# Performance work log

Hardware: AMD Instinct MI355X
Metric: run time of the kernel (lower is better)

## Reference

```python
import jax, jax.numpy as jnp
import numpy as np
import math

B, S, D = 4, 2048, 768
H = 12
DH = D // H  # 64
NEG = -1e10

def setup_inputs() -> dict:
    key = jax.random.key(0)
    ks = jax.random.split(key, 8)
    scale = 0.02
    return {
        "hidden_states": jax.random.normal(ks[0], (B, S, D), dtype=jnp.float32),
        "attention_mask": jnp.zeros((B, 1, 1, S), dtype=jnp.float32),
        "Wq": jax.random.normal(ks[1], (D, D), dtype=jnp.float32) * scale,
        "bq": jnp.zeros((D,), dtype=jnp.float32),
        "Wk": jax.random.normal(ks[2], (D, D), dtype=jnp.float32) * scale,
        "bk": jnp.zeros((D,), dtype=jnp.float32),
        "Wv": jax.random.normal(ks[3], (D, D), dtype=jnp.float32) * scale,
        "bv": jnp.zeros((D,), dtype=jnp.float32),
    }

def reference(hidden_states, attention_mask, Wq, bq, Wk, bk, Wv, bv):
    # Linear projections; note attention_mask is accepted but unused, matching the torch module.
    def split_heads(x):  # [B,S,D] -> [B,H,S,DH]
        return x.reshape(B, S, H, DH).transpose(0, 2, 1, 3)
    q = split_heads(hidden_states @ Wq + bq)
    k = split_heads(hidden_states @ Wk + bk)
    v = split_heads(hidden_states @ Wv + bv)
    scores = jnp.einsum("bhqd,bhkd->bhqk", q, k) / math.sqrt(DH)
    causal = jnp.tril(jnp.ones((S, S), dtype=bool))  # masked_fill(mask==0, -1e10)
    scores = jnp.where(causal, scores, NEG)
    probs = jax.nn.softmax(scores, axis=-1)
    # dropout prob = 0.0 (eval) -> identity
    ctx = jnp.einsum("bhqk,bhkd->bhqd", probs, v)
    return ctx.transpose(0, 2, 1, 3).reshape(B, S, D)
```

## Files before the change

### kernel.cpp

```cpp
#include <hip/hip_runtime.h>
#include <hip/hip_bf16.h>

#define B_  4
#define S_  2048
#define D_  768
#define H_  12
#define DH_ 64

typedef __bf16 bf16;
typedef __attribute__((ext_vector_type(8))) __bf16 bf16x8;
typedef __attribute__((ext_vector_type(4))) __bf16 bf16x4;
typedef __attribute__((ext_vector_type(4))) float floatx4;

__device__ __forceinline__ int chunk_off(int qt) {
    if (qt < 8)  return qt;
    if (qt < 16) return 8 + 2 * (qt - 8);
    if (qt < 24) return 24 + 3 * (qt - 16);
    return 48 + 4 * (qt - 24);
}

__global__ __launch_bounds__(256) void cvt_f32_bf16(const float* __restrict__ in,
                                                    bf16* __restrict__ out, int n4) {
    int i = blockIdx.x * 256 + threadIdx.x;
    if (i < n4) {
        float4 v = ((const float4*)in)[i];
        bf16x4 o;
        o[0] = (bf16)v.x; o[1] = (bf16)v.y; o[2] = (bf16)v.z; o[3] = (bf16)v.w;
        *(bf16x4*)(out + (size_t)i * 4) = o;
    }
}

__global__ __launch_bounds__(256) void w_transpose(const float* __restrict__ w0,
                                                   const float* __restrict__ w1,
                                                   const float* __restrict__ w2,
                                                   bf16* __restrict__ Wt)
{
    const int which = blockIdx.z;
    const float* W = (which == 0) ? w0 : (which == 1 ? w1 : w2);
    bf16* dst = Wt + (size_t)which * D_ * D_;
    __shared__ bf16 t[64 * 72];
    const int k0 = blockIdx.x * 64, n0 = blockIdx.y * 64;
    const int tid = threadIdx.x;
    {
        int r = tid >> 2;
        int c0 = (tid & 3) * 16;
        #pragma unroll
        for (int q = 0; q < 4; q++) {
            float4 v = *(const float4*)(W + (size_t)(k0 + r) * D_ + n0 + c0 + q * 4);
            t[(c0 + q * 4 + 0) * 72 + r] = (bf16)v.x;
            t[(c0 + q * 4 + 1) * 72 + r] = (bf16)v.y;
            t[(c0 + q * 4 + 2) * 72 + r] = (bf16)v.z;
            t[(c0 + q * 4 + 3) * 72 + r] = (bf16)v.w;
        }
    }
    __syncthreads();
    {
        int n = tid >> 3, seg = tid & 7;
        *(bf16x8*)(dst + (size_t)(n0 + n) * D_ + k0 + seg * 8) =
            *(const bf16x8*)(t + n * 72 + seg * 8);
        *(bf16x8*)(dst + (size_t)(n0 + n + 32) * D_ + k0 + seg * 8) =
            *(const bf16x8*)(t + (n + 32) * 72 + seg * 8);
    }
}

__global__ __launch_bounds__(256) void qkv_gemm(
    const bf16* __restrict__ Xb, const bf16* __restrict__ Wt,
    const float* __restrict__ bq, const float* __restrict__ bk,
    const float* __restrict__ bv, bf16* __restrict__ QKV)
{
    const int which = blockIdx.z;
    const bf16* Wm = Wt + (size_t)which * D_ * D_;
    const float* bias = (which == 0) ? bq : (which == 1 ? bk : bv);
    bf16* out = QKV + (size_t)which * B_ * H_ * S_ * DH_;

    __shared__ bf16 As[128 * 72];
    __shared__ bf16 Bs[128 * 72];

    const int tid  = threadIdx.x;
    const int wave = tid >> 6, lane = tid & 63;
    const int wr = wave >> 1, wc = wave & 1;
    const int g = lane >> 4, ln = lane & 15;
    const int m0 = blockIdx.x * 128, n0 = blockIdx.y * 128;

    floatx4 acc[4][4];
    #pragma unroll
    for (int i = 0; i < 4; i++)
        #pragma unroll
        for (int j = 0; j < 4; j++)
            acc[i][j] = (floatx4){0.f, 0.f, 0.f, 0.f};

    int row_[4], seg_[4];
    #pragma unroll
    for (int t = 0; t < 4; t++) { int fc = tid + t * 256; row_[t] = fc >> 3; seg_[t] = fc & 7; }

    bf16x8 apf[4], bpf[4];
    #pragma unroll
    for (int t = 0; t < 4; t++) {
        apf[t] = *(const bf16x8*)(Xb + (size_t)(m0 + row_[t]) * D_ + seg_[t] * 8);
        bpf[t] = *(const bf16x8*)(Wm + (size_t)(n0 + row_[t]) * D_ + seg_[t] * 8);
    }

    for (int k0 = 0; k0 < D_; k0 += 64) {
        __syncthreads();
        #pragma unroll
        for (int t = 0; t < 4; t++) {
            *(bf16x8*)(As + row_[t] * 72 + seg_[t] * 8) = apf[t];
            *(bf16x8*)(Bs + row_[t] * 72 + seg_[t] * 8) = bpf[t];
        }
        __syncthreads();
        if (k0 + 64 < D_) {
            #pragma unroll
            for (int t = 0; t < 4; t++) {
                apf[t] = *(const bf16x8*)(Xb + (size_t)(m0 + row_[t]) * D_ + k0 + 64 + seg_[t] * 8);
                bpf[t] = *(const bf16x8*)(Wm + (size_t)(n0 + row_[t]) * D_ + k0 + 64 + seg_[t] * 8);
            }
        }
        #pragma unroll
        for (int ks = 0; ks < 2; ks++) {
            bf16x8 af[4], bfr[4];
            #pragma unroll
            for (int i = 0; i < 4; i++)
                af[i] = *(const bf16x8*)(As + (wr * 64 + i * 16 + ln) * 72 + ks * 32 + g * 8);
            #pragma unroll
            for (int j = 0; j < 4; j++)
                bfr[j] = *(const bf16x8*)(Bs + (wc * 64 + j * 16 + ln) * 72 + ks * 32 + g * 8);
            #pragma unroll
            for (int i = 0; i < 4; i++)
                #pragma unroll
                for (int j = 0; j < 4; j++)
                    acc[i][j] = __builtin_amdgcn_mfma_f32_16x16x32_bf16(af[i], bfr[j], acc[i][j], 0, 0, 0);
        }
    }

    #pragma unroll
    for (int i = 0; i < 4; i++) {
        #pragma unroll
        for (int j = 0; j < 4; j++) {
            int col = n0 + wc * 64 + j * 16 + ln;
            float bv_ = bias[col];
            int h = col >> 6, dh = col & 63;
            int rowbase = m0 + wr * 64 + i * 16 + g * 4;
            int b = rowbase >> 11, s0 = rowbase & 2047;
            if (which == 2) {
                bf16x4 o;
                #pragma unroll
                for (int r = 0; r < 4; r++) o[r] = (bf16)(acc[i][j][r] + bv_);
                *(bf16x4*)(out + ((size_t)((b * H_ + h) * DH_ + dh)) * S_ + s0) = o;
            } else {
                #pragma unroll
                for (int r = 0; r < 4; r++)
                    out[(((size_t)(b * H_ + h) * S_ + s0 + r) << 6) + dh] =
                        (bf16)(acc[i][j][r] + bv_);
            }
        }
    }
}

__global__ __launch_bounds__(256) void attn_chunk(const bf16* __restrict__ QKV,
                                                  float* __restrict__ out,
                                                  bf16* __restrict__ Opart,
                                                  float* __restrict__ Lpart)
{
    const int cid = 79 - blockIdx.x;
    const int bh = blockIdx.y;
    const int b = bh / H_, h = bh % H_;

    int qt, c;
    if (cid < 8)       { qt = cid; c = 0; }
    else if (cid < 24) { qt = 8 + ((cid - 8) >> 1); c = (cid - 8) & 1; }
    else if (cid < 48) { int t3 = cid - 24; qt = 16 + t3 / 3; c = t3 - (qt - 16) * 3; }
    else               { int t4 = cid - 48; qt = 24 + (t4 >> 2); c = t4 & 3; }
    const int nch = (qt >> 3) + 1;
    const int kt0 = c * 8;
    const int kt1 = min(kt0 + 7, qt);

    const size_t MAT = (size_t)B_ * H_ * S_ * DH_;
    const bf16* Q  = QKV +           (size_t)bh * S_ * DH_;
    const bf16* K  = QKV + MAT +     (size_t)bh * S_ * DH_;
    const bf16* Vt = QKV + 2 * MAT + (size_t)bh * S_ * DH_;

    __shared__ bf16 Ks[64 * 72];
    __shared__ bf16 Vts[64 * 72];
    __shared__ bf16 Ps[4][16 * 72];

    const int tid  = threadIdx.x;
    const int wave = tid >> 6, lane = tid & 63;
    const int g = lane >> 4, ln = lane & 15;
    const int srow = tid >> 3, sseg = tid & 7;

    bf16x8 qf[2];
    {
        const bf16* qrow = Q + (size_t)(qt * 64 + wave * 16 + ln) * DH_;
        qf[0] = *(const bf16x8*)(qrow + g * 8);
        qf[1] = *(const bf16x8*)(qrow + 32 + g * 8);
    }

    bf16x8 ones;
    #pragma unroll
    for (int i = 0; i < 8; i++) ones[i] = (bf16)1.0f;

    floatx4 accO[4];
    #pragma unroll
    for (int j = 0; j < 4; j++) accO[j] = (floatx4){0.f, 0.f, 0.f, 0.f};
    floatx4 accL = (floatx4){0.f, 0.f, 0.f, 0.f};

    const bf16* kptr = K  + (size_t)(kt0 * 64 + srow) * DH_ + sseg * 8;
    const bf16* vptr = Vt + (size_t)srow * S_ + kt0 * 64 + sseg * 8;

    bf16x8 ka = *(const bf16x8*)kptr;
    bf16x8 kb = *(const bf16x8*)(kptr + 32 * DH_);
    bf16x8 va = *(const bf16x8*)vptr;
    bf16x8 vb = *(const bf16x8*)(vptr + (size_t)32 * S_);

    for (int kt = kt0; kt <= kt1; ++kt) {
        __syncthreads();
        *(bf16x8*)(Ks  + srow * 72 + sseg * 8) = ka;
        *(bf16x8*)(Ks  + (srow + 32) * 72 + sseg * 8) = kb;
        *(bf16x8*)(Vts + srow * 72 + sseg * 8) = va;
        *(bf16x8*)(Vts + (srow + 32) * 72 + sseg * 8) = vb;
        __syncthreads();
        if (kt < kt1) {
            kptr += 64 * DH_;
            vptr += 64;
            ka = *(const bf16x8*)kptr;
            kb = *(const bf16x8*)(kptr + 32 * DH_);
            va = *(const bf16x8*)vptr;
            vb = *(const bf16x8*)(vptr + (size_t)32 * S_);
        }

        floatx4 accS[4];
        #pragma unroll
        for (int j = 0; j < 4; j++) accS[j] = (floatx4){0.f, 0.f, 0.f, 0.f};
        #pragma unroll
        for (int j = 0; j < 4; j++) {
            #pragma unroll
            for (int cc = 0; cc < 2; cc++) {
                bf16x8 kf = *(const bf16x8*)(Ks + (j * 16 + ln) * 72 + cc * 32 + g * 8);
                accS[j] = __builtin_amdgcn_mfma_f32_16x16x32_bf16(qf[cc], kf, accS[j], 0, 0, 0);
            }
        }

        #pragma unroll
        for (int j = 0; j < 4; j++)
            #pragma unroll
            for (int r = 0; r < 4; r++)
                accS[j][r] = __expf(accS[j][r] * 0.125f);
        if (kt == qt) {
            #pragma unroll
            for (int j = 0; j < 4; j++) {
                int krow = j * 16 + ln;
                #pragma unroll
                for (int r = 0; r < 4; r++) {
                    int qrow = wave * 16 + g * 4 + r;
                    if (krow > qrow) accS[j][r] = 0.f;
                }
            }
        }

        bf16* Pw = Ps[wave];
        #pragma unroll
        for (int j = 0; j < 4; j++)
            #pragma unroll
            for (int r = 0; r < 4; r++)
                Pw[(g * 4 + r) * 72 + j * 16 + ln] = (bf16)accS[j][r];

        #pragma unroll
        for (int cc = 0; cc < 2; cc++) {
            bf16x8 pf = *(const bf16x8*)(Pw + ln * 72 + cc * 32 + g * 8);
            accL = __builtin_amdgcn_mfma_f32_16x16x32_bf16(pf, ones, accL, 0, 0, 0);
            #pragma unroll
            for (int j = 0; j < 4; j++) {
                bf16x8 vf = *(const bf16x8*)(Vts + (j * 16 + ln) * 72 + cc * 32 + g * 8);
                accO[j] = __builtin_amdgcn_mfma_f32_16x16x32_bf16(pf, vf, accO[j], 0, 0, 0);
            }
        }
    }

    if (nch == 1) {
        float inv[4];
        #pragma unroll
        for (int r = 0; r < 4; r++) inv[r] = 1.0f / accL[r];
        #pragma unroll
        for (int j = 0; j < 4; j++) {
            int dh = j * 16 + ln;
            #pragma unroll
            for (int r = 0; r < 4; r++) {
                int q = qt * 64 + wave * 16 + g * 4 + r;
                out[((size_t)(b * S_ + q)) * D_ + h * DH_ + dh] = accO[j][r] * inv[r];
            }
        }
    } else {
        const int chunk = bh * 80 + chunk_off(qt) + c;
        bf16x8 p0, p1;
        #pragma unroll
        for (int e = 0; e < 8; e++) {
            p0[e] = (bf16)accO[e >> 2][e & 3];
            p1[e] = (bf16)accO[2 + (e >> 2)][e & 3];
        }
        bf16* dst = Opart + (size_t)chunk * 4096 + tid * 16;
        *(bf16x8*)dst = p0;
        *(bf16x8*)(dst + 8) = p1;
        if (ln == 0) {
            #pragma unroll
            for (int r = 0; r < 4; r++)
                Lpart[chunk * 64 + wave * 16 + g * 4 + r] = accL[r];
        }
    }
}

__global__ __launch_bounds__(256) void attn_reduce(const bf16* __restrict__ Opart,
                                                   const float* __restrict__ Lpart,
                                                   float* __restrict__ out)
{
    const int qt = 8 + blockIdx.x;
    const int bh = blockIdx.y;
    const int b = bh / H_, h = bh % H_;
    const int nch = (qt >> 3) + 1;
    const int cb = bh * 80 + chunk_off(qt);

    const int tid  = threadIdx.x;
    const int wave = tid >> 6, lane = tid & 63;
    const int g = lane >> 4, ln = lane & 15;

    float o[16];
    #pragma unroll
    for (int e = 0; e < 16; e++) o[e] = 0.f;
    float ls[4] = {0.f, 0.f, 0.f, 0.f};

    for (int cidx = 0; cidx < nch; cidx++) {
        const bf16* p = Opart + (size_t)(cb + cidx) * 4096 + tid * 16;
        bf16x8 v0 = *(const bf16x8*)p;
        bf16x8 v1 = *(const bf16x8*)(p + 8);
        #pragma unroll
        for (int e = 0; e < 8; e++) { o[e] += (float)v0[e]; o[8 + e] += (float)v1[e]; }
        #pragma unroll
        for (int r = 0; r < 4; r++)
            ls[r] += Lpart[(cb + cidx) * 64 + wave * 16 + g * 4 + r];
    }
    float inv[4];
    #pragma unroll
    for (int r = 0; r < 4; r++) inv[r] = 1.0f / ls[r];
    #pragma unroll
    for (int j = 0; j < 4; j++) {
        int dh = j * 16 + ln;
        #pragma unroll
        for (int r = 0; r < 4; r++) {
            int q = qt * 64 + wave * 16 + g * 4 + r;
            out[((size_t)(b * S_ + q)) * D_ + h * DH_ + dh] = o[j * 4 + r] * inv[r];
        }
    }
}

extern "C" void kernel_launch(void* const* d_in, const int* in_sizes, int n_in,
                              void* d_out, int out_size, void* d_ws, size_t ws_size,
                              hipStream_t stream) {
    const float* hs = (const float*)d_in[0];
    const float* Wq = (const float*)d_in[2];
    const float* bq = (const float*)d_in[3];
    const float* Wk = (const float*)d_in[4];
    const float* bk = (const float*)d_in[5];
    const float* Wv = (const float*)d_in[6];
    const float* bv = (const float*)d_in[7];
    float* out = (float*)d_out;

    bf16* Xb    = (bf16*)d_ws;
    bf16* Wt    = Xb + (size_t)8192 * 768;
    bf16* QKV   = Wt + (size_t)3 * 768 * 768;
    bf16* Opart = QKV + (size_t)3 * B_ * H_ * S_ * DH_;
    float* Lpart = (float*)(Opart + (size_t)3840 * 4096);

    cvt_f32_bf16<<<6144, 256, 0, stream>>>(hs, Xb, 1572864);
    w_transpose<<<dim3(12, 12, 3), 256, 0, stream>>>(Wq, Wk, Wv, Wt);
    qkv_gemm<<<dim3(64, 6, 3), 256, 0, stream>>>(Xb, Wt, bq, bk, bv, QKV);
    attn_chunk<<<dim3(80, 48), 256, 0, stream>>>(QKV, out, Opart, Lpart);
    attn_reduce<<<dim3(24, 48), 256, 0, stream>>>(Opart, Lpart, out);
}
```

Before: 202.4 us.

## Keep attention probabilities in registers via transposed S and 16x16x16 MFMA

Computes S transposed (K as the A operand) so each lane's accumulator output already matches the B-operand layout of a 16x16x16 bf16 MFMA. P can then feed the PV and row-sum MFMAs straight from registers, removing the per-wave LDS round trip for P. The change also raises the occupancy hint via launch_bounds and wraps the MFMA section in s_setprio. In exchange it issues twice as many smaller MFMAs for PV, which adds instruction count.

```diff
diff --git a/kernel.cpp b/kernel.cpp
--- a/kernel.cpp
+++ b/kernel.cpp
@@ -11,6 +11,22 @@
 typedef __attribute__((ext_vector_type(8))) __bf16 bf16x8;
 typedef __attribute__((ext_vector_type(4))) __bf16 bf16x4;
 typedef __attribute__((ext_vector_type(4))) float floatx4;
+typedef __attribute__((ext_vector_type(4))) short short4v;
+
+#if defined(__has_builtin)
+#if __has_builtin(__builtin_amdgcn_mfma_f32_16x16x16bf16_1k)
+#define HAVE_MFMA16_BUILTIN 1
+#endif
+#endif
+static __device__ __forceinline__ floatx4 mfma16(short4v a, short4v b, floatx4 c) {
+#ifdef HAVE_MFMA16_BUILTIN
+    return __builtin_amdgcn_mfma_f32_16x16x16bf16_1k(a, b, c, 0, 0, 0);
+#else
+    floatx4 d = c;
+    asm("v_mfma_f32_16x16x16_bf16 %0, %1, %2, %0" : "+v"(d) : "v"(a), "v"(b));
+    return d;
+#endif
+}
 
 __device__ __forceinline__ int chunk_off(int qt) {
     if (qt < 8)  return qt;
@@ -156,10 +172,10 @@
     }
 }
 
-__global__ __launch_bounds__(256) void attn_chunk(const bf16* __restrict__ QKV,
-                                                  float* __restrict__ out,
-                                                  bf16* __restrict__ Opart,
-                                                  float* __restrict__ Lpart)
+__global__ __launch_bounds__(256, 8) void attn_chunk(const bf16* __restrict__ QKV,
+                                                     float* __restrict__ out,
+                                                     bf16* __restrict__ Opart,
+                                                     float* __restrict__ Lpart)
 {
     const int cid = 79 - blockIdx.x;
     const int bh = blockIdx.y;
@@ -181,7 +197,6 @@
 
     __shared__ bf16 Ks[64 * 72];
     __shared__ bf16 Vts[64 * 72];
-    __shared__ bf16 Ps[4][16 * 72];
 
     const int tid  = threadIdx.x;
     const int wave = tid >> 6, lane = tid & 63;
@@ -195,13 +210,11 @@
         qf[1] = *(const bf16x8*)(qrow + 32 + g * 8);
     }
 
-    bf16x8 ones;
-    #pragma unroll
-    for (int i = 0; i < 8; i++) ones[i] = (bf16)1.0f;
+    const short4v ones16 = {0x3F80, 0x3F80, 0x3F80, 0x3F80};
 
     floatx4 accO[4];
     #pragma unroll
-    for (int j = 0; j < 4; j++) accO[j] = (floatx4){0.f, 0.f, 0.f, 0.f};
+    for (int dt = 0; dt < 4; dt++) accO[dt] = (floatx4){0.f, 0.f, 0.f, 0.f};
     floatx4 accL = (floatx4){0.f, 0.f, 0.f, 0.f};
 
     const bf16* kptr = K  + (size_t)(kt0 * 64 + srow) * DH_ + sseg * 8;
@@ -228,52 +241,40 @@
             vb = *(const bf16x8*)(vptr + (size_t)32 * S_);
         }
 
-        floatx4 accS[4];
-        #pragma unroll
-        for (int j = 0; j < 4; j++) accS[j] = (floatx4){0.f, 0.f, 0.f, 0.f};
+        __builtin_amdgcn_s_setprio(1);
         #pragma unroll
         for (int j = 0; j < 4; j++) {
+            floatx4 accS = (floatx4){0.f, 0.f, 0.f, 0.f};
             #pragma unroll
             for (int cc = 0; cc < 2; cc++) {
                 bf16x8 kf = *(const bf16x8*)(Ks + (j * 16 + ln) * 72 + cc * 32 + g * 8);
-                accS[j] = __builtin_amdgcn_mfma_f32_16x16x32_bf16(qf[cc], kf, accS[j], 0, 0, 0);
-            }
-        }
-
-        #pragma unroll
-        for (int j = 0; j < 4; j++)
-            #pragma unroll
-            for (int r = 0; r < 4; r++)
-                accS[j][r] = __expf(accS[j][r] * 0.125f);
-        if (kt == qt) {
-            #pragma unroll
-            for (int j = 0; j < 4; j++) {
-                int krow = j * 16 + ln;
+                accS = __builtin_amdgcn_mfma_f32_16x16x32_bf16(kf, qf[cc], accS, 0, 0, 0);
+            }
+
+            #pragma unroll
+            for (int r = 0; r < 4; r++) accS[r] = __expf(accS[r] * 0.125f);
+            if (kt == qt) {
+                const int krow = j * 16 + g * 4;
+                const int qrow = wave * 16 + ln;
                 #pragma unroll
-                for (int r = 0; r < 4; r++) {
-                    int qrow = wave * 16 + g * 4 + r;
-                    if (krow > qrow) accS[j][r] = 0.f;
-                }
-            }
-        }
-
-        bf16* Pw = Ps[wave];
-        #pragma unroll
-        for (int j = 0; j < 4; j++)
-            #pragma unroll
-            for (int r = 0; r < 4; r++)
-                Pw[(g * 4 + r) * 72 + j * 16 + ln] = (bf16)accS[j][r];
-
-        #pragma unroll
-        for (int cc = 0; cc < 2; cc++) {
-            bf16x8 pf = *(const bf16x8*)(Pw + ln * 72 + cc * 32 + g * 8);
-            accL = __builtin_amdgcn_mfma_f32_16x16x32_bf16(pf, ones, accL, 0, 0, 0);
-            #pragma unroll
-            for (int j = 0; j < 4; j++) {
-                bf16x8 vf = *(const bf16x8*)(Vts + (j * 16 + ln) * 72 + cc * 32 + g * 8);
-                accO[j] = __builtin_amdgcn_mfma_f32_16x16x32_bf16(pf, vf, accO[j], 0, 0, 0);
-            }
-        }
+                for (int r = 0; r < 4; r++)
+                    if (krow + r > qrow) accS[r] = 0.f;
+            }
+
+            bf16x4 pa;
+            #pragma unroll
+            for (int r = 0; r < 4; r++) pa[r] = (bf16)accS[r];
+            short4v pas = __builtin_bit_cast(short4v, pa);
+
+            accL = mfma16(pas, ones16, accL);
+
+            #pragma unroll
+            for (int dt = 0; dt < 4; dt++) {
+                short4v vf = *(const short4v*)(Vts + (dt * 16 + ln) * 72 + j * 16 + g * 4);
+                accO[dt] = mfma16(pas, vf, accO[dt]);
+            }
+        }
+        __builtin_amdgcn_s_setprio(0);
     }
 
     if (nch == 1) {
@@ -281,12 +282,12 @@
         #pragma unroll
         for (int r = 0; r < 4; r++) inv[r] = 1.0f / accL[r];
         #pragma unroll
-        for (int j = 0; j < 4; j++) {
-            int dh = j * 16 + ln;
+        for (int dt = 0; dt < 4; dt++) {
+            int dh = dt * 16 + ln;
             #pragma unroll
             for (int r = 0; r < 4; r++) {
                 int q = qt * 64 + wave * 16 + g * 4 + r;
-                out[((size_t)(b * S_ + q)) * D_ + h * DH_ + dh] = accO[j][r] * inv[r];
+                out[((size_t)(b * S_ + q)) * D_ + h * DH_ + dh] = accO[dt][r] * inv[r];
             }
         }
     } else {
```

Result: slower. 319.1 us (+57.7%).
